# Kernel optimization log

Hardware: AMD Instinct MI355X
Metric: run time of the kernel (lower is better)

## Reference

```python
import jax, jax.numpy as jnp
import numpy as np

B, N, DIM = 4, 1024, 2048
H, HKV, D = 16, 4, 128          # n_heads, n_kv_heads, head_dim
CACHE = 3072                     # cached KV length
WINDOW = 2048                    # max_window_len (sliding window)
EPS = 1e-6


def setup_inputs() -> dict:
    key = jax.random.key(0)
    ks = jax.random.split(key, 10)
    x = jax.random.normal(ks[0], (B, N, DIM), dtype=jnp.float32)
    past_k = jax.random.normal(ks[1], (B, HKV, CACHE, D), dtype=jnp.float32)
    past_v = jax.random.normal(ks[2], (B, HKV, CACHE, D), dtype=jnp.float32)
    # RoPE angles for the current segment (absolute positions CACHE..CACHE+N-1),
    # matching MultiLevelRoPE 'face' level: freqs = 1/theta**(arange(0,D,2)/D)
    pos = jnp.arange(CACHE, CACHE + N, dtype=jnp.float32)
    inv_freq = 1.0 / (10000.0 ** (jnp.arange(0, D, 2, dtype=jnp.float32) / D))
    ang = pos[:, None] * inv_freq[None, :]          # [N, D//2]
    freqs_cos = jnp.cos(ang)
    freqs_sin = jnp.sin(ang)
    s = 0.02
    Wq = jax.random.normal(ks[3], (H * D, DIM), dtype=jnp.float32) * s
    Wk = jax.random.normal(ks[4], (HKV * D, DIM), dtype=jnp.float32) * s
    Wv = jax.random.normal(ks[5], (HKV * D, DIM), dtype=jnp.float32) * s
    Wo = jax.random.normal(ks[6], (DIM, H * D), dtype=jnp.float32) * s
    bo = jnp.zeros((DIM,), dtype=jnp.float32)
    wq_norm = jnp.ones((D,), dtype=jnp.float32)
    wk_norm = jnp.ones((D,), dtype=jnp.float32)
    return {"x": x, "past_k": past_k, "past_v": past_v,
            "freqs_cos": freqs_cos, "freqs_sin": freqs_sin,
            "Wq": Wq, "Wk": Wk, "Wv": Wv, "Wo": Wo, "bo": bo,
            "wq_norm": wq_norm, "wk_norm": wk_norm}


def _rms_norm(t, w):
    # torch.nn.RMSNorm over head_dim
    return t * jax.lax.rsqrt(jnp.mean(t * t, axis=-1, keepdims=True) + EPS) * w


def _rope(t, cos, sin):
    # interleaved-pair complex rotation, as in MultiLevelRoPE.apply
    # t: [B, h, N, D]; cos/sin: [N, D//2]
    t2 = t.reshape(*t.shape[:-1], D // 2, 2)
    x0, x1 = t2[..., 0], t2[..., 1]
    c = cos[None, None, :, :]
    s = sin[None, None, :, :]
    r0 = x0 * c - x1 * s
    r1 = x0 * s + x1 * c
    return jnp.stack([r0, r1], axis=-1).reshape(t.shape)


def reference(x, past_k, past_v, freqs_cos, freqs_sin,
              Wq, Wk, Wv, Wo, bo, wq_norm, wk_norm):
    # projections -> [B, h, N, D]
    q = (x @ Wq.T).reshape(B, N, H, D).transpose(0, 2, 1, 3)
    k = (x @ Wk.T).reshape(B, N, HKV, D).transpose(0, 2, 1, 3)
    v = (x @ Wv.T).reshape(B, N, HKV, D).transpose(0, 2, 1, 3)
    # qk rms_norm on head_dim
    q = _rms_norm(q, wq_norm)
    k = _rms_norm(k, wk_norm)
    # RoPE on current segment (cached K already rotated)
    q = _rope(q, freqs_cos, freqs_sin)
    k = _rope(k, freqs_cos, freqs_sin)
    # append to cache -> M = CACHE + N
    k_all = jnp.concatenate([past_k, k], axis=2)   # [B, HKV, M, D]
    v_all = jnp.concatenate([past_v, v], axis=2)
    # repeat_kv for GQA
    n_rep = H // HKV
    k_rep = jnp.repeat(k_all, n_rep, axis=1)       # [B, H, M, D]
    v_rep = jnp.repeat(v_all, n_rep, axis=1)
    M = CACHE + N
    scale = 1.0 / jnp.sqrt(jnp.asarray(D, dtype=q.dtype))
    scores = jnp.einsum('bhnd,bhmd->bhnm', q, k_rep) * scale
    # causal + sliding-window mask over absolute positions
    qpos = jnp.arange(N) + CACHE                   # [N]
    kpos = jnp.arange(M)                           # [M]
    allowed = (kpos[None, :] <= qpos[:, None]) & (qpos[:, None] - kpos[None, :] < WINDOW)
    scores = jnp.where(allowed[None, None], scores, jnp.asarray(-1e30, dtype=scores.dtype))
    probs = jax.nn.softmax(scores, axis=-1)
    attn = jnp.einsum('bhnm,bhmd->bhnd', probs, v_rep)
    attn = attn.transpose(0, 2, 1, 3).reshape(B, N, H * D)
    return attn @ Wo.T + bo
```

## Files before the change

### kernel.cpp

```cpp
#include <hip/hip_runtime.h>
#include <hip/hip_bf16.h>
#include <stdint.h>

typedef unsigned short u16;
typedef unsigned int u32;
typedef __attribute__((ext_vector_type(8))) __bf16 bfrag;
typedef __attribute__((ext_vector_type(4))) float f32x4;
typedef __attribute__((ext_vector_type(16))) float f32x16;
typedef __attribute__((ext_vector_type(4))) unsigned short u16x4;

__device__ __forceinline__ u16 f2bf(float f){
  union { float f; u32 u; } v; v.f = f;
  u32 u = v.u;
  return (u16)((u + 0x7fffu + ((u >> 16) & 1u)) >> 16);
}

__device__ __forceinline__ u32 cvtpk(float a, float b){
  u32 r; asm("v_cvt_pk_bf16_f32 %0, %1, %2" : "=v"(r) : "v"(a), "v"(b)); return r;
}
__device__ __forceinline__ void swap32(u32 &a, u32 &b){
  asm volatile("v_permlane32_swap_b32 %0, %1" : "+v"(a), "+v"(b));
}

__device__ __forceinline__ void gload_lds16(const void* g, void* l){
  __builtin_amdgcn_global_load_lds(
      (__attribute__((address_space(1))) void*)(unsigned long long)g,
      (__attribute__((address_space(3))) void*)(u32)(unsigned long long)l,
      16, 0, 0);
}

__global__ void __launch_bounds__(256) k_cvt(const float* __restrict__ s, u16* __restrict__ d, int n4){
  int i = blockIdx.x*256 + threadIdx.x;
  if (i >= n4) return;
  float4 v = ((const float4*)s)[i];
  u16x4 o; o[0]=f2bf(v.x); o[1]=f2bf(v.y); o[2]=f2bf(v.z); o[3]=f2bf(v.w);
  ((u16x4*)d)[i] = o;
}

__global__ void __launch_bounds__(256) k_past_kr(const float* __restrict__ pk, u16* __restrict__ Kr){
  __shared__ u16 TK[64][128];
  const int kc = 16 + blockIdx.x;
  const int pl = blockIdx.y;
  const int t = threadIdx.x;
  const float* src = pk + (size_t)pl*393216 + (size_t)kc*8192;
  #pragma unroll
  for (int i = 0; i < 8; ++i){
    int e = i*1024 + t*4;
    float4 v = *(const float4*)(src + e);
    u16x4 o; o[0]=f2bf(v.x); o[1]=f2bf(v.y); o[2]=f2bf(v.z); o[3]=f2bf(v.w);
    *(u16x4*)&TK[e>>7][e&127] = o;
  }
  __syncthreads();
  u16* dst = Kr + (size_t)pl*524288 + (size_t)kc*8192;
  #pragma unroll
  for (int i = 0; i < 4; ++i){
    int f = i*256 + t;
    int fhi = f >> 6, lf = f & 63;
    int row = ((f >> 9) << 5) | (lf & 31);
    int col = ((fhi & 7) << 4) | ((lf >> 5) << 3);
    bfrag v = *(const bfrag*)&TK[row][col];
    *(bfrag*)(dst + fhi*512 + lf*8) = v;
  }
}

__global__ void __launch_bounds__(256) k_past_vr(const float* __restrict__ pv, u16* __restrict__ Vr){
  __shared__ u16 T2[128][80];
  const int kc = 16 + blockIdx.x;
  const int pl = blockIdx.y;
  const int t = threadIdx.x;
  const float* src = pv + (size_t)pl*393216 + (size_t)kc*8192;
  #pragma unroll
  for (int i = 0; i < 8; ++i){
    int e = i*1024 + t*4;
    int row = e >> 7, d0 = e & 127;
    float4 v = *(const float4*)(src + e);
    T2[d0][row]   = f2bf(v.x);
    T2[d0+1][row] = f2bf(v.y);
    T2[d0+2][row] = f2bf(v.z);
    T2[d0+3][row] = f2bf(v.w);
  }
  __syncthreads();
  u16* dst = Vr + (size_t)pl*524288 + (size_t)kc*8192;
  #pragma unroll
  for (int i = 0; i < 4; ++i){
    int g = i*256 + t;
    int ghi = g >> 6, lg = g & 63;
    int d  = ((ghi & 3) << 5) | (lg & 31);
    int k0 = ((g >> 9) << 5) | (((ghi >> 2) & 1) << 4) | ((lg >> 5) << 3);
    bfrag v = *(const bfrag*)&T2[d][k0];
    *(bfrag*)(dst + ghi*512 + lg*8) = v;
  }
}

__global__ void __launch_bounds__(256) k_new_vr(const u16* __restrict__ vn, u16* __restrict__ Vr){
  __shared__ u16 T2[128][80];
  const int kcl = blockIdx.x;
  const int pl = blockIdx.y;
  const int t = threadIdx.x;
  const u16* src = vn + (size_t)pl*131072 + (size_t)kcl*8192;
  #pragma unroll
  for (int i = 0; i < 4; ++i){
    int e = i*2048 + t*8;
    int row = e >> 7, d0 = e & 127;
    union { bfrag v; u16 x[8]; } u;
    u.v = *(const bfrag*)(src + e);
    #pragma unroll
    for (int j = 0; j < 8; ++j) T2[d0+j][row] = u.x[j];
  }
  __syncthreads();
  u16* dst = Vr + (size_t)pl*524288 + (size_t)(48 + kcl)*8192;
  #pragma unroll
  for (int i = 0; i < 4; ++i){
    int g = i*256 + t;
    int ghi = g >> 6, lg = g & 63;
    int d  = ((ghi & 3) << 5) | (lg & 31);
    int k0 = ((g >> 9) << 5) | (((ghi >> 2) & 1) << 4) | ((lg >> 5) << 3);
    bfrag v = *(const bfrag*)&T2[d][k0];
    *(bfrag*)(dst + ghi*512 + lg*8) = v;
  }
}

template<int EPI>
__global__ void __launch_bounds__(256) k_gemm(
    const u16* __restrict__ A, const u16* __restrict__ Bm,
    u16* __restrict__ Cb, float* __restrict__ Cf, const float* __restrict__ bias,
    int M, int Nn, int K)
{
  __shared__ u16 lsA[2][4096];
  __shared__ u16 lsB[2][4096];
  const int t = threadIdx.x, lane = t & 63, wid = t >> 6;
  const int l15 = lane & 15, l4 = lane >> 4;
  const int wm = wid >> 1, wn = wid & 1;
  const int bn = blockIdx.x, bm = blockIdx.y;
  const u16* Ab = A + (size_t)bm*128*K;
  const u16* Bb = Bm + (size_t)bn*128*K;

  auto stage = [&](u16* ls, const u16* g, int kof){
    #pragma unroll
    for (int r = 0; r < 2; ++r){
      int row = r*64 + (t >> 2);
      int s = (t & 3) ^ ((row >> 1) & 3);
      gload_lds16(g + (size_t)row*K + kof + s*8, ls + r*2048 + wid*512);
    }
  };

  f32x4 acc[4][4] = {};
  stage(&lsA[0][0], Ab, 0);
  stage(&lsB[0][0], Bb, 0);
  const int NT = K >> 5;
  const int sl = l4 ^ ((l15 >> 1) & 3);
  const int ra0 = wm*64 + l15, rb0 = wn*64 + l15;
  for (int kt = 0; kt < NT; ++kt){
    __syncthreads();
    const int cur = kt & 1;
    if (kt + 1 < NT){
      stage(&lsA[cur ^ 1][0], Ab, (kt + 1)*32);
      stage(&lsB[cur ^ 1][0], Bb, (kt + 1)*32);
    }
    bfrag af[4], bfv[4];
    #pragma unroll
    for (int i = 0; i < 4; ++i){
      af[i]  = *(const bfrag*)&lsA[cur][(ra0 + i*16)*32 + sl*8];
      bfv[i] = *(const bfrag*)&lsB[cur][(rb0 + i*16)*32 + sl*8];
    }
    #pragma unroll
    for (int i = 0; i < 4; ++i)
      #pragma unroll
      for (int j = 0; j < 4; ++j)
        acc[i][j] = __builtin_amdgcn_mfma_f32_16x16x32_bf16(af[i], bfv[j], acc[i][j], 0, 0, 0);
  }
  const int row0 = bm*128 + wm*64, col0 = bn*128 + wn*64;
  #pragma unroll
  for (int i = 0; i < 4; ++i)
    #pragma unroll
    for (int j = 0; j < 4; ++j){
      int cc = col0 + j*16 + l15;
      float bv = (EPI == 1) ? bias[cc] : 0.f;
      #pragma unroll
      for (int r = 0; r < 4; ++r){
        int rr = row0 + i*16 + l4*4 + r;
        if (EPI == 0) Cb[(size_t)rr*Nn + cc] = f2bf(acc[i][j][r]);
        else          Cf[(size_t)rr*Nn + cc] = acc[i][j][r] + bv;
      }
    }
}

__global__ void __launch_bounds__(256) k_rmsrope(
    const u16* __restrict__ proj, const float* __restrict__ cosb, const float* __restrict__ sinb,
    const float* __restrict__ wq, const float* __restrict__ wk,
    u16* __restrict__ q_ro, u16* __restrict__ Kr, u16* __restrict__ v_new)
{
  const int bn = blockIdx.x;
  const int b = bn >> 10, n = bn & 1023;
  const int lane = threadIdx.x & 63, w = threadIdx.x >> 6;
  const int chunk = blockIdx.y*4 + w;
  const u16* src = proj + (size_t)bn*3072 + chunk*128 + lane*2;
  const u32 raw = *(const u32*)src;
  union { u32 u; float f; } a, c2;
  a.u = raw << 16; c2.u = raw & 0xffff0000u;
  float x0 = a.f, x1 = c2.f;
  if (chunk >= 20){
    int hk = chunk - 20;
    *(u32*)(v_new + ((size_t)(b*4 + hk)*1024 + n)*128 + lane*2) = raw;
    return;
  }
  float ss = x0*x0 + x1*x1;
  #pragma unroll
  for (int m = 1; m < 64; m <<= 1) ss += __shfl_xor(ss, m, 64);
  float inv = rsqrtf(ss*(1.f/128.f) + 1e-6f);
  const float* wn2 = (chunk < 16) ? wq : wk;
  x0 *= inv*wn2[lane*2]; x1 *= inv*wn2[lane*2 + 1];
  float cz = cosb[n*64 + lane], sz = sinb[n*64 + lane];
  float r0 = x0*cz - x1*sz;
  float r1 = x0*sz + x1*cz;
  if (chunk < 16){
    const float KLF = 0.127529904f;
    r0 *= KLF; r1 *= KLF;
    u32 outp = (u32)f2bf(r0) | ((u32)f2bf(r1) << 16);
    *(u32*)(q_ro + (((size_t)(b*16 + chunk)*1024 + n) << 7) + lane*2) = outp;
  } else {
    int hk = chunk - 16;
    u32 outp = (u32)f2bf(r0) | ((u32)f2bf(r1) << 16);
    int kpos = 3072 + n;
    size_t idx = (size_t)(b*4 + hk)*524288
               + (size_t)(((kpos >> 6)*16) + (((kpos >> 5) & 1)*8) + (lane >> 3))*512
               + (size_t)((((lane >> 2) & 1) << 5) | (kpos & 31))*8
               + ((2*lane) & 7);
    *(u32*)(Kr + idx) = outp;
  }
}

__global__ void __launch_bounds__(512, 4) k_attn(
    const u16* __restrict__ q_ro, const u16* __restrict__ Kr,
    const u16* __restrict__ Vr, u16* __restrict__ attn_o)
{
  __shared__ u16 smem[32768];
  __shared__ float Lsh[4][32];
  const int bid = blockIdx.x;
  const int xcd = bid & 7, idx = bid >> 3;
  const int plane = (xcd << 1) | (idx >> 5);
  const int qt = idx & 31;
  const int b = plane >> 2, hk = plane & 3;
  const int t = threadIdx.x, lane = t & 63, w = t >> 6;
  const int l31 = lane & 31, lh = lane >> 5;
  const int hf = w >> 2;
  const int hd = w & 3;
  const int h = hk*4 + hd;
  const int qbase = qt*32;

  const u16* qplane = q_ro + (size_t)(b*16 + h)*1024*128;
  const u16* kplane = Kr + (size_t)(b*4 + hk)*524288;
  const u16* vplane = Vr + (size_t)(b*4 + hk)*524288;

  bfrag qf[8];
  {
    const u16* qrow = qplane + (size_t)(qbase + l31)*128 + lh*8;
    #pragma unroll
    for (int dks = 0; dks < 8; ++dks)
      qf[dks] = *(const bfrag*)(qrow + dks*16);
  }

  const int kb0 = (qbase + 1024) & ~63;
  const int kc0 = kb0 >> 6;
  const int qpos = 3072 + qbase + l31;

  const char* smb = (const char*)smem;
  const int krd = hf*8192 + lane*16;
  const int vrd = 32768 + hf*8192 + lane*16;

  f32x16 acc_o[4] = {};
  float l_run = 0.f;

  {
    const u16* ks = kplane + (size_t)kc0*8192 + t*8;
    const u16* vs = vplane + (size_t)kc0*8192 + t*8;
    gload_lds16(ks,        smem + t*8);
    gload_lds16(ks + 4096, smem + 4096 + t*8);
    gload_lds16(vs,        smem + 16384 + t*8);
    gload_lds16(vs + 4096, smem + 20480 + t*8);
  }

  for (int c = 0; c < 33; ++c){
    __syncthreads();
    const int cur = c & 1;
    if (c < 32){
      const u16* ks = kplane + (size_t)(kc0 + c + 1)*8192 + t*8;
      const u16* vs = vplane + (size_t)(kc0 + c + 1)*8192 + t*8;
      u16* kd = smem + (cur ^ 1)*8192 + t*8;
      u16* vd = smem + 16384 + (cur ^ 1)*8192 + t*8;
      gload_lds16(ks,        kd);
      gload_lds16(ks + 4096, kd + 4096);
      gload_lds16(vs,        vd);
      gload_lds16(vs + 4096, vd + 4096);
    }

    const int kbase = krd + cur*16384;
    f32x16 s = {};
    __builtin_amdgcn_s_setprio(1);
    #pragma unroll
    for (int dks = 0; dks < 8; ++dks){
      bfrag kf = *(const bfrag*)(smb + kbase + dks*1024);
      s = __builtin_amdgcn_mfma_f32_32x32x16_bf16(kf, qf[dks], s, 0, 0, 0);
    }
    __builtin_amdgcn_s_setprio(0);

    if ((c == 0) | (c == 32)){
      const int kb = kb0 + c*64;
      #pragma unroll
      for (int r = 0; r < 16; ++r){
        int kpos = kb + hf*32 + (r & 3) + 8*(r >> 2) + 4*lh;
        int dq = qpos - kpos;
        if ((unsigned)dq >= 2048u) s[r] = -1e30f;
      }
    }

    #pragma unroll
    for (int r = 0; r < 16; ++r) s[r] = exp2f(s[r]);
    {
      float a0 = (s[0]+s[1]) + (s[2]+s[3]);
      float a1 = (s[4]+s[5]) + (s[6]+s[7]);
      float a2 = (s[8]+s[9]) + (s[10]+s[11]);
      float a3 = (s[12]+s[13]) + (s[14]+s[15]);
      float lc = (a0 + a1) + (a2 + a3);
      lc += __shfl_xor(lc, 32, 64);
      l_run += lc;
    }

    union { u32 u[4]; bfrag v; } pf[2];
    {
      u32 a0 = cvtpk(s[0],  s[1]),  a1 = cvtpk(s[2],  s[3]);
      u32 b0 = cvtpk(s[4],  s[5]),  b1 = cvtpk(s[6],  s[7]);
      swap32(a0, b0); swap32(a1, b1);
      pf[0].u[0]=a0; pf[0].u[1]=a1; pf[0].u[2]=b0; pf[0].u[3]=b1;
      u32 c0 = cvtpk(s[8],  s[9]),  c1 = cvtpk(s[10], s[11]);
      u32 e0 = cvtpk(s[12], s[13]), e1 = cvtpk(s[14], s[15]);
      swap32(c0, e0); swap32(c1, e1);
      pf[1].u[0]=c0; pf[1].u[1]=c1; pf[1].u[2]=e0; pf[1].u[3]=e1;
    }

    const int vbase = vrd + cur*16384;
    __builtin_amdgcn_s_setprio(1);
    #pragma unroll
    for (int lks = 0; lks < 2; ++lks)
      #pragma unroll
      for (int dj = 0; dj < 4; ++dj){
        bfrag vf = *(const bfrag*)(smb + vbase + (lks*4 + dj)*1024);
        acc_o[dj] = __builtin_amdgcn_mfma_f32_32x32x16_bf16(vf, pf[lks].v, acc_o[dj], 0, 0, 0);
      }
    __builtin_amdgcn_s_setprio(0);
  }

  #pragma unroll
  for (int p = 0; p < 2; ++p){
    __syncthreads();
    if (hf == 1 && (hd >> 1) == p){
      if (lh == 0) Lsh[hd][l31] = l_run;
      float* om = (float*)smem + (hd & 1)*4096;
      #pragma unroll
      for (int dj = 0; dj < 4; ++dj)
        #pragma unroll
        for (int rg = 0; rg < 4; ++rg){
          int slot = dj*8 + rg*2 + lh;
          f32x4 vv;
          #pragma unroll
          for (int j = 0; j < 4; ++j) vv[j] = acc_o[dj][rg*4 + j];
          *(f32x4*)&om[l31*128 + ((slot ^ (l31 & 7)) << 2)] = vv;
        }
    }
    __syncthreads();
    if (hf == 0 && (hd >> 1) == p){
      const float* om = (const float*)smem + (hd & 1)*4096;
      float ltot = l_run + Lsh[hd][l31];
      float inv = 1.0f / ltot;
      const int bn = b*1024 + qbase + l31;
      u16* orow = attn_o + (size_t)bn*2048 + h*128;
      #pragma unroll
      for (int dj = 0; dj < 4; ++dj)
        #pragma unroll
        for (int rg = 0; rg < 4; ++rg){
          int slot = dj*8 + rg*2 + lh;
          f32x4 vv = *(const f32x4*)&om[l31*128 + ((slot ^ (l31 & 7)) << 2)];
          int d0 = dj*32 + rg*8 + lh*4;
          u16x4 o;
          #pragma unroll
          for (int j = 0; j < 4; ++j) o[j] = f2bf((acc_o[dj][rg*4 + j] + vv[j])*inv);
          *(u16x4*)(orow + d0) = o;
        }
    }
  }
}

extern "C" void kernel_launch(void* const* d_in, const int* in_sizes, int n_in,
                              void* d_out, int out_size, void* d_ws, size_t ws_size,
                              hipStream_t stream)
{
  const float* x      = (const float*)d_in[0];
  const float* past_k = (const float*)d_in[1];
  const float* past_v = (const float*)d_in[2];
  const float* fcos   = (const float*)d_in[3];
  const float* fsin   = (const float*)d_in[4];
  const float* Wq     = (const float*)d_in[5];
  const float* Wk     = (const float*)d_in[6];
  const float* Wv     = (const float*)d_in[7];
  const float* Wo     = (const float*)d_in[8];
  const float* bo     = (const float*)d_in[9];
  const float* wqn    = (const float*)d_in[10];
  const float* wkn    = (const float*)d_in[11];
  float* out = (float*)d_out;
  char* ws = (char*)d_ws;

  u16* xb    = (u16*)(ws);
  u16* wqkv  = (u16*)(ws + 16777216);
  u16* wo_b  = (u16*)(ws + 29360128);
  u16* q_ro  = (u16*)(ws + 37748736);
  u16* Kr    = (u16*)(ws + 54525952);
  u16* Vr    = (u16*)(ws + 71303168);
  u16* v_new = (u16*)(ws + 88080384);
  u16* proj  = (u16*)(ws + 92274688);
  u16* attn_o = proj;

  k_cvt<<<8192, 256, 0, stream>>>(x, xb, 2097152);
  k_cvt<<<4096, 256, 0, stream>>>(Wq, wqkv, 1048576);
  k_cvt<<<1024, 256, 0, stream>>>(Wk, wqkv + 2048*2048, 262144);
  k_cvt<<<1024, 256, 0, stream>>>(Wv, wqkv + 2560*2048, 262144);
  k_cvt<<<4096, 256, 0, stream>>>(Wo, wo_b, 1048576);
  k_past_kr<<<dim3(32, 16), 256, 0, stream>>>(past_k, Kr);
  k_past_vr<<<dim3(32, 16), 256, 0, stream>>>(past_v, Vr);

  k_gemm<0><<<dim3(24, 32), 256, 0, stream>>>(xb, wqkv, proj, nullptr, nullptr, 4096, 3072, 2048);
  k_rmsrope<<<dim3(4096, 6), 256, 0, stream>>>(proj, fcos, fsin, wqn, wkn, q_ro, Kr, v_new);
  k_new_vr<<<dim3(16, 16), 256, 0, stream>>>(v_new, Vr);
  k_attn<<<512, 512, 0, stream>>>(q_ro, Kr, Vr, attn_o);
  k_gemm<1><<<dim3(16, 32), 256, 0, stream>>>(attn_o, wo_b, nullptr, out, bo, 4096, 2048, 2048);
}
```

Measured before the change: 260.1 us.

## Software-pipeline attention loop: compute next QK^T before current softmax and PV

Restructures the attention main loop so that the QK^T MFMAs for chunk c+1 are issued before the exp/convert/PV work of chunk c, with K staged two chunks ahead and V one chunk ahead. Two score accumulators alternate across an unrolled-by-two loop, and V fragments are preloaded into registers. The aim is to overlap the exp2 and conversion VALU work with matrix-core work. The extra live registers (a second f32x16 and eight V fragments) lead to lowering the launch bound from 4 to 2 waves per SIMD, which reduces occupancy.

```diff
diff --git a/kernel.cpp b/kernel.cpp
--- a/kernel.cpp
+++ b/kernel.cpp
@@ -230,7 +230,7 @@
   }
 }
 
-__global__ void __launch_bounds__(512, 4) k_attn(
+__global__ void __launch_bounds__(512, 2) k_attn(
     const u16* __restrict__ q_ro, const u16* __restrict__ Kr,
     const u16* __restrict__ Vr, u16* __restrict__ attn_o)
 {
@@ -268,41 +268,58 @@
   const int krd = hf*8192 + lane*16;
   const int vrd = 32768 + hf*8192 + lane*16;
 
+  auto stageK = [&](int c2, int buf){
+    const u16* ks = kplane + (size_t)(kc0 + c2)*8192 + t*8;
+    gload_lds16(ks,        smem + buf*8192 + t*8);
+    gload_lds16(ks + 4096, smem + buf*8192 + 4096 + t*8);
+  };
+  auto stageV = [&](int c2, int buf){
+    const u16* vs = vplane + (size_t)(kc0 + c2)*8192 + t*8;
+    gload_lds16(vs,        smem + 16384 + buf*8192 + t*8);
+    gload_lds16(vs + 4096, smem + 16384 + buf*8192 + 4096 + t*8);
+  };
+
   f32x16 acc_o[4] = {};
   float l_run = 0.f;
 
+  stageK(0, 0); stageK(1, 1); stageV(0, 0);
+  __syncthreads();
+
+  f32x16 sA, sB;
   {
-    const u16* ks = kplane + (size_t)kc0*8192 + t*8;
-    const u16* vs = vplane + (size_t)kc0*8192 + t*8;
-    gload_lds16(ks,        smem + t*8);
-    gload_lds16(ks + 4096, smem + 4096 + t*8);
-    gload_lds16(vs,        smem + 16384 + t*8);
-    gload_lds16(vs + 4096, smem + 20480 + t*8);
-  }
-
-  for (int c = 0; c < 33; ++c){
+    #pragma unroll
+    for (int r = 0; r < 16; ++r) sA[r] = 0.f;
+    __builtin_amdgcn_s_setprio(1);
+    #pragma unroll
+    for (int dks = 0; dks < 8; ++dks){
+      bfrag kf = *(const bfrag*)(smb + krd + dks*1024);
+      sA = __builtin_amdgcn_mfma_f32_32x32x16_bf16(kf, qf[dks], sA, 0, 0, 0);
+    }
+    __builtin_amdgcn_s_setprio(0);
+  }
+
+  auto body = [&](int c, f32x16& sCur, f32x16& sNxt){
     __syncthreads();
-    const int cur = c & 1;
+    if (c <= 30) stageK(c + 2, c & 1);
+    if (c <= 31) stageV(c + 1, (c + 1) & 1);
+
     if (c < 32){
-      const u16* ks = kplane + (size_t)(kc0 + c + 1)*8192 + t*8;
-      const u16* vs = vplane + (size_t)(kc0 + c + 1)*8192 + t*8;
-      u16* kd = smem + (cur ^ 1)*8192 + t*8;
-      u16* vd = smem + 16384 + (cur ^ 1)*8192 + t*8;
-      gload_lds16(ks,        kd);
-      gload_lds16(ks + 4096, kd + 4096);
-      gload_lds16(vs,        vd);
-      gload_lds16(vs + 4096, vd + 4096);
-    }
-
-    const int kbase = krd + cur*16384;
-    f32x16 s = {};
-    __builtin_amdgcn_s_setprio(1);
-    #pragma unroll
-    for (int dks = 0; dks < 8; ++dks){
-      bfrag kf = *(const bfrag*)(smb + kbase + dks*1024);
-      s = __builtin_amdgcn_mfma_f32_32x32x16_bf16(kf, qf[dks], s, 0, 0, 0);
-    }
-    __builtin_amdgcn_s_setprio(0);
+      #pragma unroll
+      for (int r = 0; r < 16; ++r) sNxt[r] = 0.f;
+      const int kbase = krd + ((c + 1) & 1)*16384;
+      __builtin_amdgcn_s_setprio(1);
+      #pragma unroll
+      for (int dks = 0; dks < 8; ++dks){
+        bfrag kf = *(const bfrag*)(smb + kbase + dks*1024);
+        sNxt = __builtin_amdgcn_mfma_f32_32x32x16_bf16(kf, qf[dks], sNxt, 0, 0, 0);
+      }
+      __builtin_amdgcn_s_setprio(0);
+    }
+
+    bfrag vf[8];
+    const int vbase = vrd + (c & 1)*16384;
+    #pragma unroll
+    for (int g = 0; g < 8; ++g) vf[g] = *(const bfrag*)(smb + vbase + g*1024);
 
     if ((c == 0) | (c == 32)){
       const int kb = kb0 + c*64;
@@ -310,17 +327,17 @@
       for (int r = 0; r < 16; ++r){
         int kpos = kb + hf*32 + (r & 3) + 8*(r >> 2) + 4*lh;
         int dq = qpos - kpos;
-        if ((unsigned)dq >= 2048u) s[r] = -1e30f;
+        if ((unsigned)dq >= 2048u) sCur[r] = -1e30f;
       }
     }
 
     #pragma unroll
-    for (int r = 0; r < 16; ++r) s[r] = exp2f(s[r]);
+    for (int r = 0; r < 16; ++r) sCur[r] = exp2f(sCur[r]);
     {
-      float a0 = (s[0]+s[1]) + (s[2]+s[3]);
-      float a1 = (s[4]+s[5]) + (s[6]+s[7]);
-      float a2 = (s[8]+s[9]) + (s[10]+s[11]);
-      float a3 = (s[12]+s[13]) + (s[14]+s[15]);
+      float a0 = (sCur[0]+sCur[1]) + (sCur[2]+sCur[3]);
+      float a1 = (sCur[4]+sCur[5]) + (sCur[6]+sCur[7]);
+      float a2 = (sCur[8]+sCur[9]) + (sCur[10]+sCur[11]);
+      float a3 = (sCur[12]+sCur[13]) + (sCur[14]+sCur[15]);
       float lc = (a0 + a1) + (a2 + a3);
       lc += __shfl_xor(lc, 32, 64);
       l_run += lc;
@@ -328,27 +345,31 @@
 
     union { u32 u[4]; bfrag v; } pf[2];
     {
-      u32 a0 = cvtpk(s[0],  s[1]),  a1 = cvtpk(s[2],  s[3]);
-      u32 b0 = cvtpk(s[4],  s[5]),  b1 = cvtpk(s[6],  s[7]);
+      u32 a0 = cvtpk(sCur[0],  sCur[1]),  a1 = cvtpk(sCur[2],  sCur[3]);
+      u32 b0 = cvtpk(sCur[4],  sCur[5]),  b1 = cvtpk(sCur[6],  sCur[7]);
       swap32(a0, b0); swap32(a1, b1);
       pf[0].u[0]=a0; pf[0].u[1]=a1; pf[0].u[2]=b0; pf[0].u[3]=b1;
-      u32 c0 = cvtpk(s[8],  s[9]),  c1 = cvtpk(s[10], s[11]);
-      u32 e0 = cvtpk(s[12], s[13]), e1 = cvtpk(s[14], s[15]);
+      u32 c0 = cvtpk(sCur[8],  sCur[9]),  c1 = cvtpk(sCur[10], sCur[11]);
+      u32 e0 = cvtpk(sCur[12], sCur[13]), e1 = cvtpk(sCur[14], sCur[15]);
       swap32(c0, e0); swap32(c1, e1);
       pf[1].u[0]=c0; pf[1].u[1]=c1; pf[1].u[2]=e0; pf[1].u[3]=e1;
     }
 
-    const int vbase = vrd + cur*16384;
     __builtin_amdgcn_s_setprio(1);
     #pragma unroll
     for (int lks = 0; lks < 2; ++lks)
       #pragma unroll
-      for (int dj = 0; dj < 4; ++dj){
-        bfrag vf = *(const bfrag*)(smb + vbase + (lks*4 + dj)*1024);
-        acc_o[dj] = __builtin_amdgcn_mfma_f32_32x32x16_bf16(vf, pf[lks].v, acc_o[dj], 0, 0, 0);
-      }
+      for (int dj = 0; dj < 4; ++dj)
+        acc_o[dj] = __builtin_amdgcn_mfma_f32_32x32x16_bf16(vf[lks*4 + dj], pf[lks].v, acc_o[dj], 0, 0, 0);
     __builtin_amdgcn_s_setprio(0);
-  }
+  };
+
+  #pragma unroll 1
+  for (int cc = 0; cc < 16; ++cc){
+    body(2*cc,     sA, sB);
+    body(2*cc + 1, sB, sA);
+  }
+  body(32, sA, sB);
 
   #pragma unroll
   for (int p = 0; p < 2; ++p){
```

Measured after the change: 255.4 us (median of 3 runs). No clear change (-1.8%).
